# Performance work log

Measured on AMD Instinct MI355X. Metric: run time of the kernel, lower is better.

Reference implementation:

```python
import jax, jax.numpy as jnp
import numpy as np
import math

C = 512
HEADS = 8
GROUPS = 32
HIDDEN = C * 4
EPS = 1e-5


def group_norm(x, gamma, beta, groups, eps=EPS):
    # x: (b, c, *spatial). Normalize per (sample, group) over (c//g, *spatial).
    b, c = x.shape[0], x.shape[1]
    xg = x.reshape(b, groups, -1)
    mean = xg.mean(axis=-1, keepdims=True)
    var = xg.var(axis=-1, keepdims=True)
    xg = (xg - mean) * jax.lax.rsqrt(var + eps)
    xn = xg.reshape(x.shape)
    shape = (1, c) + (1,) * (x.ndim - 2)
    return xn * gamma.reshape(shape) + beta.reshape(shape)


def setup_inputs() -> dict:
    key = jax.random.key(0)
    ks = jax.random.split(key, 10)
    s = lambda fan_in: 1.0 / math.sqrt(fan_in)
    inp = {
        "x": jax.random.normal(ks[0], (8, C, 32, 32), dtype=jnp.float32),
        "gn1_gamma": jnp.ones((C,), jnp.float32),
        "gn1_beta": jnp.zeros((C,), jnp.float32),
        "qkv_w": jax.random.uniform(ks[1], (3 * C, C), jnp.float32, -s(C), s(C)),
        "qkv_b": jax.random.uniform(ks[2], (3 * C,), jnp.float32, -s(C), s(C)),
        "out_w": jax.random.uniform(ks[3], (C, C), jnp.float32, -s(C), s(C)),
        "out_b": jax.random.uniform(ks[4], (C,), jnp.float32, -s(C), s(C)),
        "gn2_gamma": jnp.ones((C,), jnp.float32),
        "gn2_beta": jnp.zeros((C,), jnp.float32),
        "mlp1_w": jax.random.uniform(ks[5], (2 * HIDDEN, C), jnp.float32, -s(C), s(C)),
        "mlp2_w": jax.random.uniform(ks[6], (C, HIDDEN), jnp.float32, -s(HIDDEN), s(HIDDEN)),
    }
    return inp


def reference(x, gn1_gamma, gn1_beta, qkv_w, qkv_b, out_w, out_b,
              gn2_gamma, gn2_beta, mlp1_w, mlp2_w):
    b, c, h, w = x.shape
    n = h * w
    head_dim = c // HEADS
    x_norm = group_norm(x, gn1_gamma, gn1_beta, GROUPS).reshape(b, c, n)
    # 1x1 conv1d == channel matmul
    qkv = jnp.einsum('oc,bcn->bon', qkv_w, x_norm) + qkv_b[None, :, None]
    q, k, v = jnp.split(qkv, 3, axis=1)
    split_heads = lambda t: t.reshape(b, HEADS, head_dim, n).transpose(0, 1, 3, 2)  # b h n d
    q, k, v = split_heads(q), split_heads(k), split_heads(v)
    attn = jnp.einsum('bhnd,bhmd->bhnm', q, k) / math.sqrt(head_dim)
    attn = jax.nn.softmax(attn, axis=-1)  # internally max-stabilized
    x_attn = jnp.einsum('bhnm,bhmd->bhnd', attn, v)
    x_attn = x_attn.transpose(0, 1, 3, 2).reshape(b, c, n)  # b (h d) n
    x_attn = jnp.einsum('oc,bcn->bon', out_w, x_attn) + out_b[None, :, None]
    x_attn = group_norm(x_attn, gn2_gamma, gn2_beta, GROUPS)
    x_attn = x_attn.transpose(0, 2, 1)  # b n c
    hgate = x_attn @ mlp1_w.T  # b n 2*hidden
    h1, gate = jnp.split(hgate, 2, axis=-1)
    x_attn = jax.nn.silu(h1) * gate
    x_attn = x_attn @ mlp2_w.T  # b n c
    x_attn = x_attn.transpose(0, 2, 1).reshape(b, c, h, w)
    return x + x_attn
```

## Files before the change

kernel.cpp:

```cpp
#include <hip/hip_runtime.h>

typedef unsigned short ushort_t;
typedef __bf16 bf16x8 __attribute__((ext_vector_type(8)));
typedef float f32x4 __attribute__((ext_vector_type(4)));
typedef unsigned short u16x8 __attribute__((ext_vector_type(8)));
typedef unsigned short u16x4 __attribute__((ext_vector_type(4)));
typedef unsigned int __attribute__((address_space(1))) as1_uint;
typedef unsigned int __attribute__((address_space(3))) as3_uint;

#define DEV __device__ __forceinline__

DEV float bf2f(ushort_t u) { union { float f; unsigned i; } c; c.i = (unsigned)u << 16; return c.f; }
DEV ushort_t f2bf(float f) {
  union { float f; unsigned i; } c; c.f = f;
  return (ushort_t)((c.i + 0x7FFFu + ((c.i >> 16) & 1u)) >> 16);
}

DEV f32x4 mfma16(bf16x8 a, bf16x8 b, f32x4 c) {
  return __builtin_amdgcn_mfma_f32_16x16x32_bf16(a, b, c, 0, 0, 0);
}

DEV void g2lds16(const void* g, void* l) {
  __builtin_amdgcn_global_load_lds((as1_uint*)g, (as3_uint*)l, 16, 0, 0);
}

__global__ __launch_bounds__(256) void cvt_all(const float* __restrict__ w0, const float* __restrict__ w1,
                                               const float* __restrict__ w2, const float* __restrict__ w3,
                                               ushort_t* __restrict__ o0, ushort_t* __restrict__ o1,
                                               ushort_t* __restrict__ o2, ushort_t* __restrict__ o3) {
  int i = blockIdx.x * 256 + threadIdx.x;
  const float* src; ushort_t* dst; int base;
  if (i < 196608)      { src = w0; dst = o0; base = 0; }
  else if (i < 262144) { src = w1; dst = o1; base = 196608; }
  else if (i < 786432) { src = w2; dst = o2; base = 262144; }
  else                 { src = w3; dst = o3; base = 786432; }
  int j = i - base;
  float4 v = ((const float4*)src)[j];
  u16x4 o;
  o[0] = f2bf(v.x); o[1] = f2bf(v.y); o[2] = f2bf(v.z); o[3] = f2bf(v.w);
  ((u16x4*)dst)[j] = o;
}

__global__ __launch_bounds__(256) void gn_stats_cn(const float* __restrict__ x, float* __restrict__ st) {
  int b = blockIdx.x >> 5, g = blockIdx.x & 31;
  const float4* base = (const float4*)(x + ((size_t)b * 512 + g * 16) * 1024);
  float s = 0.f, sq = 0.f;
  for (int i = threadIdx.x; i < 4096; i += 256) {
    float4 v = base[i];
    s += v.x + v.y + v.z + v.w;
    sq += v.x * v.x + v.y * v.y + v.z * v.z + v.w * v.w;
  }
  #pragma unroll
  for (int mk = 1; mk < 64; mk <<= 1) { s += __shfl_xor(s, mk); sq += __shfl_xor(sq, mk); }
  __shared__ float red[8];
  if ((threadIdx.x & 63) == 0) { red[(threadIdx.x >> 6) * 2] = s; red[(threadIdx.x >> 6) * 2 + 1] = sq; }
  __syncthreads();
  if (threadIdx.x == 0) {
    s = red[0] + red[2] + red[4] + red[6];
    sq = red[1] + red[3] + red[5] + red[7];
    float mean = s * (1.f / 16384.f);
    float var = sq * (1.f / 16384.f) - mean * mean;
    st[blockIdx.x * 2] = mean;
    st[blockIdx.x * 2 + 1] = rsqrtf(var + 1e-5f);
  }
}

__global__ __launch_bounds__(256) void gn_stats_nc(const ushort_t* __restrict__ OP, float* __restrict__ st) {
  int b = blockIdx.x >> 5, g = blockIdx.x & 31;
  float s = 0.f, sq = 0.f;
  for (int jj = threadIdx.x; jj < 2048; jj += 256) {
    int n = jj >> 1, c8 = (jj & 1) * 8;
    u16x8 v = *(const u16x8*)(OP + (size_t)(b * 1024 + n) * 512 + g * 16 + c8);
    #pragma unroll
    for (int t = 0; t < 8; ++t) { float f = bf2f(v[t]); s += f; sq += f * f; }
  }
  #pragma unroll
  for (int mk = 1; mk < 64; mk <<= 1) { s += __shfl_xor(s, mk); sq += __shfl_xor(sq, mk); }
  __shared__ float red[8];
  if ((threadIdx.x & 63) == 0) { red[(threadIdx.x >> 6) * 2] = s; red[(threadIdx.x >> 6) * 2 + 1] = sq; }
  __syncthreads();
  if (threadIdx.x == 0) {
    s = red[0] + red[2] + red[4] + red[6];
    sq = red[1] + red[3] + red[5] + red[7];
    float mean = s * (1.f / 16384.f);
    float var = sq * (1.f / 16384.f) - mean * mean;
    st[blockIdx.x * 2] = mean;
    st[blockIdx.x * 2 + 1] = rsqrtf(var + 1e-5f);
  }
}

__global__ __launch_bounds__(256) void gn1_norm_t(const float* __restrict__ x, const float* __restrict__ st,
                                                  const float* __restrict__ gamma, const float* __restrict__ beta,
                                                  ushort_t* __restrict__ XN) {
  __shared__ float tile[64][65];
  int b = blockIdx.z, c0 = blockIdx.y * 64, n0 = blockIdx.x * 64;
  int tx = threadIdx.x & 63, ty = threadIdx.x >> 6;
  for (int i = ty; i < 64; i += 4) {
    int c = c0 + i;
    float mean = st[(b * 32 + (c >> 4)) * 2], rstd = st[(b * 32 + (c >> 4)) * 2 + 1];
    float v = x[((size_t)b * 512 + c) * 1024 + n0 + tx];
    tile[i][tx] = (v - mean) * rstd * gamma[c] + beta[c];
  }
  __syncthreads();
  for (int j = ty; j < 64; j += 4)
    XN[(size_t)(b * 1024 + n0 + j) * 512 + c0 + tx] = f2bf(tile[tx][j]);
}

__global__ __launch_bounds__(256) void transpose_v(const ushort_t* __restrict__ QKVT, ushort_t* __restrict__ VT) {
  __shared__ ushort_t tile[64][65];
  int b = blockIdx.z, c0 = blockIdx.y * 64, n0 = blockIdx.x * 64;
  int tx = threadIdx.x & 63, ty = threadIdx.x >> 6;
  for (int j = ty; j < 64; j += 4)
    tile[j][tx] = QKVT[(size_t)(b * 1024 + n0 + j) * 1536 + 1024 + c0 + tx];
  __syncthreads();
  for (int i = ty; i < 64; i += 4)
    VT[((size_t)b * 512 + c0 + i) * 1024 + n0 + tx] = tile[tx][i];
}

__global__ __launch_bounds__(256) void gn2_norm(const ushort_t* __restrict__ OP, const float* __restrict__ st,
                                                const float* __restrict__ gamma, const float* __restrict__ beta,
                                                ushort_t* __restrict__ XN2) {
  size_t idx = ((size_t)blockIdx.x * 256 + threadIdx.x) * 8;
  int c0 = (int)(idx & 511);
  int gi = (int)(idx >> 9);
  int b = gi >> 10;
  int g = c0 >> 4;
  float mean = st[(b * 32 + g) * 2], rstd = st[(b * 32 + g) * 2 + 1];
  u16x8 v = *(const u16x8*)(OP + idx);
  u16x8 o;
  #pragma unroll
  for (int t = 0; t < 8; ++t) {
    int c = c0 + t;
    o[t] = f2bf((bf2f(v[t]) - mean) * rstd * gamma[c] + beta[c]);
  }
  *(u16x8*)(XN2 + idx) = o;
}

template <int EPI>
__global__ __launch_bounds__(256) void gemm_bt(const ushort_t* __restrict__ A, int lda,
                                               const ushort_t* __restrict__ B, int ldb,
                                               const float* __restrict__ bias,
                                               void* __restrict__ Out, int ldo, int K,
                                               const float* __restrict__ resid) {
  constexpr int NJ = 2;
  constexpr int BN = NJ * 32;
  __shared__ __align__(16) ushort_t As[2][128 * 64];
  __shared__ __align__(16) ushort_t Bs[2][BN * 64];
  const int tid = threadIdx.x;
  const int lane = tid & 63, wave = tid >> 6;
  const int l15 = lane & 15, l4 = lane >> 4;
  const int m0 = blockIdx.y * 128, n0 = blockIdx.x * BN;
  const int wr = (wave >> 1) * 64, wc = (wave & 1) * (NJ * 16);
  const int sx = l15 & 7;
  f32x4 acc[4][NJ] = {};

  auto stage = [&](int bufi, int kk) {
    #pragma unroll
    for (int p = 0; p < 4; ++p) {
      int s = p * 256 + wave * 64 + lane;
      int row = s >> 3, c8 = ((s & 7) ^ (row & 7)) * 8;
      g2lds16(A + (size_t)(m0 + row) * lda + kk + c8, (char*)As[bufi] + (p * 256 + wave * 64) * 16);
    }
    #pragma unroll
    for (int p = 0; p < NJ; ++p) {
      int s = p * 256 + wave * 64 + lane;
      int row = s >> 3, c8 = ((s & 7) ^ (row & 7)) * 8;
      g2lds16(B + (size_t)(n0 + row) * ldb + kk + c8, (char*)Bs[bufi] + (p * 256 + wave * 64) * 16);
    }
  };
  auto compute = [&](int bufi) {
    const ushort_t* Asb = As[bufi];
    const ushort_t* Bsb = Bs[bufi];
    #pragma unroll
    for (int ks = 0; ks < 2; ++ks) {
      const int co = ((ks * 4 + l4) ^ sx) << 3;
      bf16x8 af[4], bfr[NJ];
      #pragma unroll
      for (int i = 0; i < 4; ++i)
        af[i] = *(const bf16x8*)(Asb + (wr + i * 16 + l15) * 64 + co);
      #pragma unroll
      for (int j = 0; j < NJ; ++j)
        bfr[j] = *(const bf16x8*)(Bsb + (wc + j * 16 + l15) * 64 + co);
      #pragma unroll
      for (int i = 0; i < 4; ++i)
        #pragma unroll
        for (int j = 0; j < NJ; ++j)
          acc[i][j] = mfma16(af[i], bfr[j], acc[i][j]);
    }
  };

  stage(0, 0);
  asm volatile("s_waitcnt vmcnt(0)" ::: "memory");
  __builtin_amdgcn_s_barrier();
  int cur = 0;
  for (int k0 = 0; k0 < K; k0 += 64) {
    if (k0 + 64 < K) {
      stage(cur ^ 1, k0 + 64);
      asm volatile("s_waitcnt vmcnt(6)" ::: "memory");
    } else {
      asm volatile("s_waitcnt vmcnt(0)" ::: "memory");
    }
    __builtin_amdgcn_s_barrier();
    compute(cur);
    __builtin_amdgcn_s_barrier();
    cur ^= 1;
  }

  #pragma unroll
  for (int i = 0; i < 4; ++i) {
    #pragma unroll
    for (int j = 0; j < NJ; ++j) {
      int row = m0 + wr + i * 16 + l4 * 4;
      int col = n0 + wc + j * 16 + l15;
      if constexpr (EPI == 0) {
        float bv = bias ? bias[col] : 0.f;
        ushort_t* o = (ushort_t*)Out;
        #pragma unroll
        for (int r = 0; r < 4; ++r)
          o[(size_t)(row + r) * ldo + col] = f2bf(acc[i][j][r] + bv);
      } else {
        int bb = row >> 10, n = row & 1023;
        size_t idx = ((size_t)bb * 512 + col) * 1024 + n;
        float4 rv = *(const float4*)(resid + idx);
        float4 ov = make_float4(acc[i][j][0] + rv.x, acc[i][j][1] + rv.y,
                                acc[i][j][2] + rv.z, acc[i][j][3] + rv.w);
        *(float4*)((float*)Out + idx) = ov;
      }
    }
  }
}

__global__ __launch_bounds__(256) void gemm_mlp1(const ushort_t* __restrict__ A,
                                                 const ushort_t* __restrict__ B1,
                                                 const ushort_t* __restrict__ B2,
                                                 ushort_t* __restrict__ Out) {
  __shared__ __align__(16) ushort_t As[2][128 * 64];
  __shared__ __align__(16) ushort_t B1s[2][64 * 64];
  __shared__ __align__(16) ushort_t B2s[2][64 * 64];
  const int tid = threadIdx.x;
  const int lane = tid & 63, wave = tid >> 6;
  const int l15 = lane & 15, l4 = lane >> 4;
  const int m0 = blockIdx.y * 128, n0 = blockIdx.x * 64;
  const int wr = (wave >> 1) * 64, wc = (wave & 1) * 32;
  const int sx = l15 & 7;
  f32x4 acc1[4][2] = {};
  f32x4 acc2[4][2] = {};

  auto stage = [&](int bufi, int kk) {
    #pragma unroll
    for (int p = 0; p < 4; ++p) {
      int s = p * 256 + wave * 64 + lane;
      int row = s >> 3, c8 = ((s & 7) ^ (row & 7)) * 8;
      g2lds16(A + (size_t)(m0 + row) * 512 + kk + c8, (char*)As[bufi] + (p * 256 + wave * 64) * 16);
    }
    #pragma unroll
    for (int p = 0; p < 2; ++p) {
      int s = p * 256 + wave * 64 + lane;
      int row = s >> 3, c8 = ((s & 7) ^ (row & 7)) * 8;
      g2lds16(B1 + (size_t)(n0 + row) * 512 + kk + c8, (char*)B1s[bufi] + (p * 256 + wave * 64) * 16);
      g2lds16(B2 + (size_t)(n0 + row) * 512 + kk + c8, (char*)B2s[bufi] + (p * 256 + wave * 64) * 16);
    }
  };
  auto compute = [&](int bufi) {
    const ushort_t* Asb = As[bufi];
    const ushort_t* B1b = B1s[bufi];
    const ushort_t* B2b = B2s[bufi];
    #pragma unroll
    for (int ks = 0; ks < 2; ++ks) {
      const int co = ((ks * 4 + l4) ^ sx) << 3;
      bf16x8 af[4], b1f[2], b2f[2];
      #pragma unroll
      for (int i = 0; i < 4; ++i)
        af[i] = *(const bf16x8*)(Asb + (wr + i * 16 + l15) * 64 + co);
      #pragma unroll
      for (int j = 0; j < 2; ++j) {
        b1f[j] = *(const bf16x8*)(B1b + (wc + j * 16 + l15) * 64 + co);
        b2f[j] = *(const bf16x8*)(B2b + (wc + j * 16 + l15) * 64 + co);
      }
      #pragma unroll
      for (int i = 0; i < 4; ++i)
        #pragma unroll
        for (int j = 0; j < 2; ++j) {
          acc1[i][j] = mfma16(af[i], b1f[j], acc1[i][j]);
          acc2[i][j] = mfma16(af[i], b2f[j], acc2[i][j]);
        }
    }
  };

  stage(0, 0);
  asm volatile("s_waitcnt vmcnt(0)" ::: "memory");
  __builtin_amdgcn_s_barrier();
  int cur = 0;
  for (int k0 = 0; k0 < 512; k0 += 64) {
    if (k0 + 64 < 512) {
      stage(cur ^ 1, k0 + 64);
      asm volatile("s_waitcnt vmcnt(8)" ::: "memory");
    } else {
      asm volatile("s_waitcnt vmcnt(0)" ::: "memory");
    }
    __builtin_amdgcn_s_barrier();
    compute(cur);
    __builtin_amdgcn_s_barrier();
    cur ^= 1;
  }

  #pragma unroll
  for (int i = 0; i < 4; ++i) {
    #pragma unroll
    for (int j = 0; j < 2; ++j) {
      int row = m0 + wr + i * 16 + l4 * 4;
      int col = n0 + wc + j * 16 + l15;
      #pragma unroll
      for (int r = 0; r < 4; ++r) {
        float h1 = acc1[i][j][r];
        float sg = h1 / (1.f + __expf(-h1));
        Out[(size_t)(row + r) * 2048 + col] = f2bf(sg * acc2[i][j][r]);
      }
    }
  }
}

__global__ __launch_bounds__(512, 4) void attn_kernel(const ushort_t* __restrict__ QKVT,
                                                      const ushort_t* __restrict__ VT,
                                                      ushort_t* __restrict__ AT) {
  __shared__ __align__(16) ushort_t Kt[2][64 * 64];
  __shared__ __align__(16) ushort_t Vt[2][64 * 64];
  __shared__ __align__(16) ushort_t Pl[8][16 * 64];
  const int tid = threadIdx.x, lane = tid & 63, wave = tid >> 6;
  const int l15 = lane & 15, l4 = lane >> 4;
  const int b = blockIdx.x >> 3, h = blockIdx.x & 7;
  const int qr0 = blockIdx.y * 128 + wave * 16;
  bf16x8 qf[2];
  #pragma unroll
  for (int ks = 0; ks < 2; ++ks)
    qf[ks] = *(const bf16x8*)(QKVT + (size_t)(b * 1024 + qr0 + l15) * 1536 + h * 64 + ks * 32 + l4 * 8);
  f32x4 acc_o[4] = {};
  float lsum[4] = {0.f, 0.f, 0.f, 0.f};
  const float scale = 0.125f;

  auto stage = [&](int bufi, int m0) {
    int s = tid;
    int row = s >> 3, c8 = ((s & 7) ^ (row & 7)) * 8;
    g2lds16(QKVT + (size_t)(b * 1024 + m0 + row) * 1536 + 512 + h * 64 + c8,
            (char*)Kt[bufi] + (wave * 64) * 16);
    g2lds16(VT + ((size_t)b * 512 + h * 64 + row) * 1024 + m0 + c8,
            (char*)Vt[bufi] + (wave * 64) * 16);
  };

  stage(0, 0);
  asm volatile("s_waitcnt vmcnt(0)" ::: "memory");
  __builtin_amdgcn_s_barrier();
  int cur = 0;
  #pragma unroll 1
  for (int t = 0; t < 16; ++t) {
    if (t < 15) {
      stage(cur ^ 1, (t + 1) * 64);
      asm volatile("s_waitcnt vmcnt(2)" ::: "memory");
    } else {
      asm volatile("s_waitcnt vmcnt(0)" ::: "memory");
    }
    __builtin_amdgcn_s_barrier();
    const ushort_t* Ktb = Kt[cur];
    const ushort_t* Vtb = Vt[cur];
    f32x4 accs[4] = {};
    __builtin_amdgcn_s_setprio(1);
    #pragma unroll
    for (int ks = 0; ks < 2; ++ks) {
      #pragma unroll
      for (int j = 0; j < 4; ++j) {
        bf16x8 kf = *(const bf16x8*)(Ktb + (j * 16 + l15) * 64 + (((ks * 4 + l4) ^ (l15 & 7)) << 3));
        accs[j] = mfma16(qf[ks], kf, accs[j]);
      }
    }
    __builtin_amdgcn_s_setprio(0);
    #pragma unroll
    for (int j = 0; j < 4; ++j)
      #pragma unroll
      for (int r = 0; r < 4; ++r) {
        float pv = __expf(accs[j][r] * scale);
        accs[j][r] = pv;
        lsum[r] += pv;
      }
    #pragma unroll
    for (int j = 0; j < 4; ++j)
      #pragma unroll
      for (int r = 0; r < 4; ++r) {
        int prow = l4 * 4 + r, pcol = j * 16 + l15;
        Pl[wave][prow * 64 + ((((pcol >> 3) ^ (prow & 7)) << 3) | (pcol & 7))] = f2bf(accs[j][r]);
      }
    __builtin_amdgcn_s_setprio(1);
    #pragma unroll
    for (int km = 0; km < 2; ++km) {
      bf16x8 pf = *(const bf16x8*)(&Pl[wave][l15 * 64 + (((km * 4 + l4) ^ (l15 & 7)) << 3)]);
      #pragma unroll
      for (int jd = 0; jd < 4; ++jd) {
        bf16x8 vf = *(const bf16x8*)(Vtb + (jd * 16 + l15) * 64 + (((km * 4 + l4) ^ (l15 & 7)) << 3));
        acc_o[jd] = mfma16(pf, vf, acc_o[jd]);
      }
    }
    __builtin_amdgcn_s_setprio(0);
    __builtin_amdgcn_s_barrier();
    cur ^= 1;
  }
  #pragma unroll
  for (int mk = 1; mk < 16; mk <<= 1)
    #pragma unroll
    for (int r = 0; r < 4; ++r)
      lsum[r] += __shfl_xor(lsum[r], mk);
  float inv[4];
  #pragma unroll
  for (int r = 0; r < 4; ++r) inv[r] = 1.f / lsum[r];
  #pragma unroll
  for (int jd = 0; jd < 4; ++jd)
    #pragma unroll
    for (int r = 0; r < 4; ++r)
      AT[(size_t)(b * 1024 + qr0 + l4 * 4 + r) * 512 + h * 64 + jd * 16 + l15] =
          f2bf(acc_o[jd][r] * inv[r]);
}

extern "C" void kernel_launch(void* const* d_in, const int* in_sizes, int n_in,
                              void* d_out, int out_size, void* d_ws, size_t ws_size,
                              hipStream_t stream) {
  const float* x    = (const float*)d_in[0];
  const float* g1   = (const float*)d_in[1];
  const float* b1   = (const float*)d_in[2];
  const float* qkvw = (const float*)d_in[3];
  const float* qkvb = (const float*)d_in[4];
  const float* outw = (const float*)d_in[5];
  const float* outb = (const float*)d_in[6];
  const float* g2   = (const float*)d_in[7];
  const float* b2   = (const float*)d_in[8];
  const float* m1w  = (const float*)d_in[9];
  const float* m2w  = (const float*)d_in[10];

  char* ws = (char*)d_ws;
  const size_t MB = 1ull << 20;
  ushort_t* XN   = (ushort_t*)(ws + 0);
  ushort_t* QKVT = (ushort_t*)(ws + 8 * MB);
  ushort_t* VT   = (ushort_t*)(ws + 32 * MB);
  ushort_t* AT   = (ushort_t*)(ws + 40 * MB);
  ushort_t* OP   = (ushort_t*)(ws + 48 * MB);
  ushort_t* XN2  = (ushort_t*)(ws + 0);
  ushort_t* HID  = (ushort_t*)(ws + 8 * MB);
  ushort_t* WQ   = (ushort_t*)(ws + 88 * MB);
  ushort_t* WO   = (ushort_t*)(ws + 90 * MB);
  ushort_t* WM1  = (ushort_t*)(ws + 91 * MB);
  ushort_t* WM2  = (ushort_t*)(ws + 96 * MB);
  float*    ST1  = (float*)(ws + 99 * MB);
  float*    ST2  = (float*)(ws + 99 * MB + 4096);

  cvt_all<<<4096, 256, 0, stream>>>(qkvw, outw, m1w, m2w, WQ, WO, WM1, WM2);

  gn_stats_cn<<<256, 256, 0, stream>>>(x, ST1);
  gn1_norm_t<<<dim3(16, 8, 8), 256, 0, stream>>>(x, ST1, g1, b1, XN);

  gemm_bt<0><<<dim3(24, 64), 256, 0, stream>>>(XN, 512, WQ, 512, qkvb, QKVT, 1536, 512, nullptr);
  transpose_v<<<dim3(16, 8, 8), 256, 0, stream>>>(QKVT, VT);
  attn_kernel<<<dim3(64, 8), 512, 0, stream>>>(QKVT, VT, AT);

  gemm_bt<0><<<dim3(8, 64), 256, 0, stream>>>(AT, 512, WO, 512, outb, OP, 512, 512, nullptr);
  gn_stats_nc<<<256, 256, 0, stream>>>(OP, ST2);
  gn2_norm<<<2048, 256, 0, stream>>>(OP, ST2, g2, b2, XN2);

  gemm_mlp1<<<dim3(32, 64), 256, 0, stream>>>(XN2, WM1, WM1 + 2048 * 512, HID);

  gemm_bt<1><<<dim3(8, 64), 256, 0, stream>>>(HID, 2048, WM2, 2048, nullptr, d_out, 0, 2048, x);
}
```

Baseline: 275.2 us.

## Fuse V transpose into QKV GEMM epilogue and use 8 waves in MLP1 GEMM

The QKV projection GEMM gets a new epilogue mode that writes Q/K columns row-major as before but stores V columns directly in transposed (b, c, n) layout. This removes the separate transpose_v kernel and its extra read and write of V. Separately, the gated MLP1 GEMM moves from 256 to 512 threads, with each wave owning a 32x32 sub-tile instead of 64x32. B1 and B2 staging is split between wave halves and the vmcnt wait is adjusted to match. This raises waves per block and lowers per-wave accumulator registers, at the cost of less register reuse per wave and more LDS fragment reads.

```diff
diff --git a/kernel.cpp b/kernel.cpp
--- a/kernel.cpp
+++ b/kernel.cpp
@@ -106,17 +106,6 @@
     XN[(size_t)(b * 1024 + n0 + j) * 512 + c0 + tx] = f2bf(tile[tx][j]);
 }
 
-__global__ __launch_bounds__(256) void transpose_v(const ushort_t* __restrict__ QKVT, ushort_t* __restrict__ VT) {
-  __shared__ ushort_t tile[64][65];
-  int b = blockIdx.z, c0 = blockIdx.y * 64, n0 = blockIdx.x * 64;
-  int tx = threadIdx.x & 63, ty = threadIdx.x >> 6;
-  for (int j = ty; j < 64; j += 4)
-    tile[j][tx] = QKVT[(size_t)(b * 1024 + n0 + j) * 1536 + 1024 + c0 + tx];
-  __syncthreads();
-  for (int i = ty; i < 64; i += 4)
-    VT[((size_t)b * 512 + c0 + i) * 1024 + n0 + tx] = tile[tx][i];
-}
-
 __global__ __launch_bounds__(256) void gn2_norm(const ushort_t* __restrict__ OP, const float* __restrict__ st,
                                                 const float* __restrict__ gamma, const float* __restrict__ beta,
                                                 ushort_t* __restrict__ XN2) {
@@ -141,7 +130,8 @@
                                                const ushort_t* __restrict__ B, int ldb,
                                                const float* __restrict__ bias,
                                                void* __restrict__ Out, int ldo, int K,
-                                               const float* __restrict__ resid) {
+                                               const float* __restrict__ resid,
+                                               ushort_t* __restrict__ vt) {
   constexpr int NJ = 2;
   constexpr int BN = NJ * 32;
   __shared__ __align__(16) ushort_t As[2][128 * 64];
@@ -218,19 +208,33 @@
         #pragma unroll
         for (int r = 0; r < 4; ++r)
           o[(size_t)(row + r) * ldo + col] = f2bf(acc[i][j][r] + bv);
-      } else {
+      } else if constexpr (EPI == 1) {
         int bb = row >> 10, n = row & 1023;
         size_t idx = ((size_t)bb * 512 + col) * 1024 + n;
         float4 rv = *(const float4*)(resid + idx);
         float4 ov = make_float4(acc[i][j][0] + rv.x, acc[i][j][1] + rv.y,
                                 acc[i][j][2] + rv.z, acc[i][j][3] + rv.w);
         *(float4*)((float*)Out + idx) = ov;
-      }
-    }
-  }
-}
-
-__global__ __launch_bounds__(256) void gemm_mlp1(const ushort_t* __restrict__ A,
+      } else {
+        float bv = bias[col];
+        if (col < 1024) {
+          ushort_t* o = (ushort_t*)Out;
+          #pragma unroll
+          for (int r = 0; r < 4; ++r)
+            o[(size_t)(row + r) * ldo + col] = f2bf(acc[i][j][r] + bv);
+        } else {
+          int bb = row >> 10, n = row & 1023;
+          u16x4 pk;
+          #pragma unroll
+          for (int r = 0; r < 4; ++r) pk[r] = f2bf(acc[i][j][r] + bv);
+          *(u16x4*)(vt + ((size_t)(bb * 512 + col - 1024)) * 1024 + n) = pk;
+        }
+      }
+    }
+  }
+}
+
+__global__ __launch_bounds__(512) void gemm_mlp1(const ushort_t* __restrict__ A,
                                                  const ushort_t* __restrict__ B1,
                                                  const ushort_t* __restrict__ B2,
                                                  ushort_t* __restrict__ Out) {
@@ -241,24 +245,25 @@
   const int lane = tid & 63, wave = tid >> 6;
   const int l15 = lane & 15, l4 = lane >> 4;
   const int m0 = blockIdx.y * 128, n0 = blockIdx.x * 64;
-  const int wr = (wave >> 1) * 64, wc = (wave & 1) * 32;
+  const int wm = wave & 3, wn = wave >> 2;
   const int sx = l15 & 7;
-  f32x4 acc1[4][2] = {};
-  f32x4 acc2[4][2] = {};
+  f32x4 acc1[2][2] = {};
+  f32x4 acc2[2][2] = {};
 
   auto stage = [&](int bufi, int kk) {
     #pragma unroll
-    for (int p = 0; p < 4; ++p) {
-      int s = p * 256 + wave * 64 + lane;
+    for (int p = 0; p < 2; ++p) {
+      int s = p * 512 + tid;
       int row = s >> 3, c8 = ((s & 7) ^ (row & 7)) * 8;
-      g2lds16(A + (size_t)(m0 + row) * 512 + kk + c8, (char*)As[bufi] + (p * 256 + wave * 64) * 16);
-    }
+      g2lds16(A + (size_t)(m0 + row) * 512 + kk + c8, (char*)As[bufi] + (p * 512 + wave * 64) * 16);
+    }
+    const ushort_t* Bp = (wave < 4) ? B1 : B2;
+    char* dbase = (wave < 4) ? (char*)B1s[bufi] : (char*)B2s[bufi];
     #pragma unroll
     for (int p = 0; p < 2; ++p) {
-      int s = p * 256 + wave * 64 + lane;
+      int s = p * 256 + (tid & 255);
       int row = s >> 3, c8 = ((s & 7) ^ (row & 7)) * 8;
-      g2lds16(B1 + (size_t)(n0 + row) * 512 + kk + c8, (char*)B1s[bufi] + (p * 256 + wave * 64) * 16);
-      g2lds16(B2 + (size_t)(n0 + row) * 512 + kk + c8, (char*)B2s[bufi] + (p * 256 + wave * 64) * 16);
+      g2lds16(Bp + (size_t)(n0 + row) * 512 + kk + c8, dbase + (p * 256 + (wave & 3) * 64) * 16);
     }
   };
   auto compute = [&](int bufi) {
@@ -268,17 +273,17 @@
     #pragma unroll
     for (int ks = 0; ks < 2; ++ks) {
       const int co = ((ks * 4 + l4) ^ sx) << 3;
-      bf16x8 af[4], b1f[2], b2f[2];
-      #pragma unroll
-      for (int i = 0; i < 4; ++i)
-        af[i] = *(const bf16x8*)(Asb + (wr + i * 16 + l15) * 64 + co);
+      bf16x8 af[2], b1f[2], b2f[2];
+      #pragma unroll
+      for (int i = 0; i < 2; ++i)
+        af[i] = *(const bf16x8*)(Asb + (wm * 32 + i * 16 + l15) * 64 + co);
       #pragma unroll
       for (int j = 0; j < 2; ++j) {
-        b1f[j] = *(const bf16x8*)(B1b + (wc + j * 16 + l15) * 64 + co);
-        b2f[j] = *(const bf16x8*)(B2b + (wc + j * 16 + l15) * 64 + co);
-      }
-      #pragma unroll
-      for (int i = 0; i < 4; ++i)
+        b1f[j] = *(const bf16x8*)(B1b + (wn * 32 + j * 16 + l15) * 64 + co);
+        b2f[j] = *(const bf16x8*)(B2b + (wn * 32 + j * 16 + l15) * 64 + co);
+      }
+      #pragma unroll
+      for (int i = 0; i < 2; ++i)
         #pragma unroll
         for (int j = 0; j < 2; ++j) {
           acc1[i][j] = mfma16(af[i], b1f[j], acc1[i][j]);
@@ -294,7 +299,7 @@
   for (int k0 = 0; k0 < 512; k0 += 64) {
     if (k0 + 64 < 512) {
       stage(cur ^ 1, k0 + 64);
-      asm volatile("s_waitcnt vmcnt(8)" ::: "memory");
+      asm volatile("s_waitcnt vmcnt(4)" ::: "memory");
     } else {
       asm volatile("s_waitcnt vmcnt(0)" ::: "memory");
     }
@@ -305,11 +310,11 @@
   }
 
   #pragma unroll
-  for (int i = 0; i < 4; ++i) {
+  for (int i = 0; i < 2; ++i) {
     #pragma unroll
     for (int j = 0; j < 2; ++j) {
-      int row = m0 + wr + i * 16 + l4 * 4;
-      int col = n0 + wc + j * 16 + l15;
+      int row = m0 + wm * 32 + i * 16 + l4 * 4;
+      int col = n0 + wn * 32 + j * 16 + l15;
       #pragma unroll
       for (int r = 0; r < 4; ++r) {
         float h1 = acc1[i][j][r];
@@ -454,15 +459,14 @@
   gn_stats_cn<<<256, 256, 0, stream>>>(x, ST1);
   gn1_norm_t<<<dim3(16, 8, 8), 256, 0, stream>>>(x, ST1, g1, b1, XN);
 
-  gemm_bt<0><<<dim3(24, 64), 256, 0, stream>>>(XN, 512, WQ, 512, qkvb, QKVT, 1536, 512, nullptr);
-  transpose_v<<<dim3(16, 8, 8), 256, 0, stream>>>(QKVT, VT);
+  gemm_bt<2><<<dim3(24, 64), 256, 0, stream>>>(XN, 512, WQ, 512, qkvb, QKVT, 1536, 512, nullptr, VT);
   attn_kernel<<<dim3(64, 8), 512, 0, stream>>>(QKVT, VT, AT);
 
-  gemm_bt<0><<<dim3(8, 64), 256, 0, stream>>>(AT, 512, WO, 512, outb, OP, 512, 512, nullptr);
+  gemm_bt<0><<<dim3(8, 64), 256, 0, stream>>>(AT, 512, WO, 512, outb, OP, 512, 512, nullptr, nullptr);
   gn_stats_nc<<<256, 256, 0, stream>>>(OP, ST2);
   gn2_norm<<<2048, 256, 0, stream>>>(OP, ST2, g2, b2, XN2);
 
-  gemm_mlp1<<<dim3(32, 64), 256, 0, stream>>>(XN2, WM1, WM1 + 2048 * 512, HID);
-
-  gemm_bt<1><<<dim3(8, 64), 256, 0, stream>>>(HID, 2048, WM2, 2048, nullptr, d_out, 0, 2048, x);
-}
+  gemm_mlp1<<<dim3(32, 64), 512, 0, stream>>>(XN2, WM1, WM1 + 2048 * 512, HID);
+
+  gemm_bt<1><<<dim3(8, 64), 256, 0, stream>>>(HID, 2048, WM2, 2048, nullptr, d_out, 0, 2048, x, nullptr);
+}
```

Result: faster. 268.3 us (-2.5%).
